# Kernel optimization log

Hardware: AMD Instinct MI355X
Metric: run time of the kernel (lower is better)

Reference implementation:

```python
import jax, jax.numpy as jnp
import numpy as np

TARGET_LEN = 288
HIDDEN = 128
INPUT_SIZE = 7
OUT_SIZE = 3  # len(quantiles)
BATCH = 1024
SEQ = 288


def _lstm_cell(x_t, h, c, Wih, Whh, b):
    # PyTorch LSTM gate order: i, f, g, o; z: (B, 4H)
    z = x_t @ Wih.T + h @ Whh.T + b
    i, f, g, o = jnp.split(z, 4, axis=-1)
    c_new = jax.nn.sigmoid(f) * c + jax.nn.sigmoid(i) * jnp.tanh(g)
    h_new = jax.nn.sigmoid(o) * jnp.tanh(c_new)
    return h_new, c_new


def setup_inputs() -> dict:
    key = jax.random.key(0)
    ks = jax.random.split(key, 11)
    s = 0.08  # ~ 1/sqrt(hidden), matches torch LSTM uniform init scale
    return {
        "x": jax.random.normal(ks[0], (BATCH, SEQ, INPUT_SIZE), jnp.float32),
        "enc_Wih": jax.random.normal(ks[1], (4 * HIDDEN, INPUT_SIZE), jnp.float32) * s,
        "enc_Whh": jax.random.normal(ks[2], (4 * HIDDEN, HIDDEN), jnp.float32) * s,
        "enc_bih": jax.random.normal(ks[3], (4 * HIDDEN,), jnp.float32) * s,
        "enc_bhh": jax.random.normal(ks[4], (4 * HIDDEN,), jnp.float32) * s,
        "dec_Wih": jax.random.normal(ks[5], (4 * HIDDEN, OUT_SIZE), jnp.float32) * s,
        "dec_Whh": jax.random.normal(ks[6], (4 * HIDDEN, HIDDEN), jnp.float32) * s,
        "dec_bih": jax.random.normal(ks[7], (4 * HIDDEN,), jnp.float32) * s,
        "dec_bhh": jax.random.normal(ks[8], (4 * HIDDEN,), jnp.float32) * s,
        "out_W": jax.random.normal(ks[9], (OUT_SIZE, HIDDEN), jnp.float32) * s,
        "out_b": jax.random.normal(ks[10], (OUT_SIZE,), jnp.float32) * s,
    }


def reference(x, enc_Wih, enc_Whh, enc_bih, enc_bhh,
              dec_Wih, dec_Whh, dec_bih, dec_bhh, out_W, out_b):
    B = x.shape[0]
    H = enc_Whh.shape[1]
    b_enc = enc_bih + enc_bhh
    b_dec = dec_bih + dec_bhh

    # ----- encoder LSTM over the input sequence -----
    def enc_step(carry, x_t):
        h, c = carry
        h, c = _lstm_cell(x_t, h, c, enc_Wih, enc_Whh, b_enc)
        return (h, c), None

    h0 = jnp.zeros((B, H), x.dtype)
    (h_enc, c_enc), _ = jax.lax.scan(enc_step, (h0, h0), jnp.swapaxes(x, 0, 1))

    # returned state, so every step restarts from (h_enc, c_enc); only the
    # previous output (quantiles) feeds back. Dropout is identity (eval). -----
    def dec_step(y_prev, _):
        h, _c = _lstm_cell(y_prev, h_enc, c_enc, dec_Wih, dec_Whh, b_dec)
        y = h @ out_W.T + out_b  # (B, OUT_SIZE)
        return y, y

    y0 = jnp.zeros((B, out_W.shape[0]), x.dtype)
    _, ys = jax.lax.scan(dec_step, y0, None, length=TARGET_LEN)  # (T, B, O)
    return jnp.swapaxes(ys, 0, 1)  # (B, TARGET_LEN, OUT_SIZE)
```

## Files before the change

### kernel.cpp

```cpp
#include <hip/hip_runtime.h>

#define SEQ 288
#define INP 7
#define HID 128
#define TLEN 288
#define OUTD 3
#define XW (SEQ * INP)

typedef _Float16 f16x8 __attribute__((ext_vector_type(8)));
typedef float f32x4 __attribute__((ext_vector_type(4)));

#define NLOG2E  (-1.4426950408889634f)
#define N2LOG2E (-2.8853900817779268f)

__device__ __forceinline__ float exp2_fast(float x) {
#if __has_builtin(__builtin_amdgcn_exp2f)
    return __builtin_amdgcn_exp2f(x);
#else
    return __expf(x * 0.69314718056f);
#endif
}
__device__ __forceinline__ float sig2(float zp) {
    return __builtin_amdgcn_rcpf(1.0f + exp2_fast(zp));
}
__device__ __forceinline__ float tanh2(float zp) {
    return 2.0f * __builtin_amdgcn_rcpf(1.0f + exp2_fast(zp)) - 1.0f;
}

template<int CTRL, int RM>
__device__ __forceinline__ float dpp_add(float v) {
    int t = __builtin_amdgcn_update_dpp(0, __float_as_int(v), CTRL, RM, 0xF, true);
    return v + __int_as_float(t);
}
__device__ __forceinline__ float wave_sum(float v) {
    v = dpp_add<0xB1, 0xF>(v);
    v = dpp_add<0x4E, 0xF>(v);
    v = dpp_add<0x124, 0xF>(v);
    v = dpp_add<0x128, 0xF>(v);
    v = dpp_add<0x142, 0xA>(v);
    v = dpp_add<0x143, 0xC>(v);
    return __int_as_float(__builtin_amdgcn_readlane(__float_as_int(v), 63));
}

__device__ __forceinline__ float sel4(f32x4 s, bool m1, bool m2) {
    float a = m1 ? s[1] : s[0];
    float b = m1 ? s[3] : s[2];
    return m2 ? b : a;
}

__global__ __launch_bounds__(512, 2)
void enc_dec_kernel(const float* __restrict__ x,
                    const float* __restrict__ eWih, const float* __restrict__ eWhh,
                    const float* __restrict__ ebih, const float* __restrict__ ebhh,
                    const float* __restrict__ dWih, const float* __restrict__ dWhh,
                    const float* __restrict__ dbih, const float* __restrict__ dbhh,
                    const float* __restrict__ oW,  const float* __restrict__ ob,
                    float* __restrict__ out)
{
    __shared__ __align__(16) _Float16 hbuf[2][4][4][40];
    __shared__ __align__(16) _Float16 xf16[SEQ + 1][4][8];
    __shared__ float zbl[4][4][HID];
    __shared__ float cl[4][HID];

    const int tid  = threadIdx.x;
    const int wave = tid >> 6;
    const int lane = tid & 63;
    const int col  = lane & 15;
    const int grp  = lane >> 4;
    const int u    = wave * 16 + col;
    const int bb   = grp;
    const int b0   = blockIdx.x * 4;
    const bool m1  = (grp & 1) != 0;
    const bool m2  = (grp & 2) != 0;

    const float GS[4] = {NLOG2E, NLOG2E, N2LOG2E, NLOG2E};

    {
        _Float16* hb = &hbuf[0][0][0][0];
        for (int i = tid; i < 2 * 4 * 4 * 40; i += 512) hb[i] = (_Float16)0.f;
        _Float16* xp = &xf16[SEQ][0][0];
        if (tid < 32) xp[tid] = (_Float16)0.f;
    }
    for (int i = tid; i < 4 * XW; i += 512) {
        int b = i / XW, r = i % XW;
        int t = r / INP, j = r % INP;
        xf16[t][b][j] = (_Float16)x[(size_t)(b0 + b) * XW + r];
    }
    for (int i = tid; i < SEQ * 4; i += 512)
        xf16[i >> 2][i & 3][7] = (_Float16)1.0f;

    f16x8 wfrag[4][5];
    #pragma unroll
    for (int gt = 0; gt < 4; ++gt) {
        const int row = gt * HID + u;
        const float gs = GS[gt];
        #pragma unroll
        for (int kc = 0; kc < 4; ++kc) {
            const float* wr = eWhh + (size_t)row * HID + kc * 32 + grp * 8;
            f16x8 wf;
            #pragma unroll
            for (int e = 0; e < 8; ++e) wf[e] = (_Float16)(gs * wr[e]);
            wfrag[gt][kc] = wf;
        }
        {
            f16x8 wf;
            #pragma unroll
            for (int e = 0; e < 8; ++e) {
                int j = grp * 8 + e;
                float v = 0.f;
                if (j < INP)       v = eWih[(size_t)row * INP + j];
                else if (j == 7)   v = ebih[row] + ebhh[row];
                wf[e] = (_Float16)(gs * v);
            }
            wfrag[gt][4] = wf;
        }
    }

    __syncthreads();

    float cc = 0.f;
    const f32x4 zero = (f32x4){0.f, 0.f, 0.f, 0.f};

    f32x4 accX[4];
    {
        f16x8 ax0 = *(const f16x8*)&xf16[0][col & 3][0];
        #pragma unroll
        for (int gt = 0; gt < 4; ++gt)
            accX[gt] = __builtin_amdgcn_mfma_f32_16x16x32_f16(ax0, wfrag[gt][4], zero, 0, 0, 0);
    }

    #define ENC_STEP(T, CUR, NXT)                                                     \
    {                                                                                 \
        f16x8 af0 = *(const f16x8*)&hbuf[CUR][0][col & 3][grp * 8];                   \
        f16x8 af1 = *(const f16x8*)&hbuf[CUR][1][col & 3][grp * 8];                   \
        f16x8 af2 = *(const f16x8*)&hbuf[CUR][2][col & 3][grp * 8];                   \
        f16x8 af3 = *(const f16x8*)&hbuf[CUR][3][col & 3][grp * 8];                   \
        f32x4 acc[4];                                                                 \
        _Pragma("unroll")                                                             \
        for (int gt = 0; gt < 4; ++gt) {                                              \
            acc[gt] = __builtin_amdgcn_mfma_f32_16x16x32_f16(af0, wfrag[gt][0], accX[gt], 0, 0, 0); \
            acc[gt] = __builtin_amdgcn_mfma_f32_16x16x32_f16(af1, wfrag[gt][1], acc[gt], 0, 0, 0);  \
            acc[gt] = __builtin_amdgcn_mfma_f32_16x16x32_f16(af2, wfrag[gt][2], acc[gt], 0, 0, 0);  \
            acc[gt] = __builtin_amdgcn_mfma_f32_16x16x32_f16(af3, wfrag[gt][3], acc[gt], 0, 0, 0);  \
        }                                                                             \
        f16x8 axn = *(const f16x8*)&xf16[(T) + 1][col & 3][0];                        \
        _Pragma("unroll")                                                             \
        for (int gt = 0; gt < 4; ++gt)                                                \
            accX[gt] = __builtin_amdgcn_mfma_f32_16x16x32_f16(axn, wfrag[gt][4], zero, 0, 0, 0);    \
        float zi = sel4(acc[0], m1, m2);                                              \
        float zf = sel4(acc[1], m1, m2);                                              \
        float zg = sel4(acc[2], m1, m2);                                              \
        float zo = sel4(acc[3], m1, m2);                                              \
        float si = sig2(zi);                                                          \
        float sf = sig2(zf);                                                          \
        float tg = tanh2(zg);                                                         \
        float so = sig2(zo);                                                          \
        cc = sf * cc + si * tg;                                                       \
        float h = so * tanh2(cc * N2LOG2E);                                           \
        hbuf[NXT][u >> 5][bb][u & 31] = (_Float16)h;                                  \
        __syncthreads();                                                              \
    }

    for (int t = 0; t < SEQ; t += 2) {
        ENC_STEP(t, 0, 1)
        ENC_STEP(t + 1, 1, 0)
    }
    #undef ENC_STEP

    #pragma unroll
    for (int gt = 0; gt < 4; ++gt) {
        const int row = gt * HID + u;
        const float gs = GS[gt];
        #pragma unroll
        for (int kc = 0; kc < 4; ++kc) {
            const float* wr = dWhh + (size_t)row * HID + kc * 32 + grp * 8;
            f16x8 wf;
            #pragma unroll
            for (int e = 0; e < 8; ++e) wf[e] = (_Float16)(gs * wr[e]);
            wfrag[gt][kc] = wf;
        }
    }
    {
        f16x8 af0 = *(const f16x8*)&hbuf[0][0][col & 3][grp * 8];
        f16x8 af1 = *(const f16x8*)&hbuf[0][1][col & 3][grp * 8];
        f16x8 af2 = *(const f16x8*)&hbuf[0][2][col & 3][grp * 8];
        f16x8 af3 = *(const f16x8*)&hbuf[0][3][col & 3][grp * 8];
        #pragma unroll
        for (int gt = 0; gt < 4; ++gt) {
            float bd = GS[gt] * (dbih[gt * HID + u] + dbhh[gt * HID + u]);
            f32x4 acc = (f32x4){bd, bd, bd, bd};
            acc = __builtin_amdgcn_mfma_f32_16x16x32_f16(af0, wfrag[gt][0], acc, 0, 0, 0);
            acc = __builtin_amdgcn_mfma_f32_16x16x32_f16(af1, wfrag[gt][1], acc, 0, 0, 0);
            acc = __builtin_amdgcn_mfma_f32_16x16x32_f16(af2, wfrag[gt][2], acc, 0, 0, 0);
            acc = __builtin_amdgcn_mfma_f32_16x16x32_f16(af3, wfrag[gt][3], acc, 0, 0, 0);
            zbl[gt][bb][u] = sel4(acc, m1, m2);
        }
        cl[bb][u] = cc;
    }
    __syncthreads();

    if (wave >= 4) return;
    {
        const int b = wave;
        const int u0 = lane, u1 = 64 + lane;
        float zb0[4], zb1[4], wd0[4][3], wd1[4][3];
        #pragma unroll
        for (int gt = 0; gt < 4; ++gt) {
            zb0[gt] = zbl[gt][b][u0];
            zb1[gt] = zbl[gt][b][u1];
            #pragma unroll
            for (int j = 0; j < 3; ++j) {
                wd0[gt][j] = GS[gt] * dWih[(size_t)(gt * HID + u0) * 3 + j];
                wd1[gt][j] = GS[gt] * dWih[(size_t)(gt * HID + u1) * 3 + j];
            }
        }
        const float c0 = cl[b][u0], c1 = cl[b][u1];
        float ow0[3], ow1[3];
        #pragma unroll
        for (int j = 0; j < 3; ++j) {
            ow0[j] = oW[j * HID + u0];
            ow1[j] = oW[j * HID + u1];
        }
        const float ob0 = ob[0], ob1 = ob[1], ob2 = ob[2];

        float y0 = 0.f, y1 = 0.f, y2 = 0.f;
        float* orow = out + (size_t)(b0 + b) * (TLEN * OUTD);

        for (int t = 0; t < TLEN; ++t) {
            float z0[4], z1[4];
            #pragma unroll
            for (int gt = 0; gt < 4; ++gt) {
                z0[gt] = zb0[gt] + wd0[gt][0] * y0 + wd0[gt][1] * y1 + wd0[gt][2] * y2;
                z1[gt] = zb1[gt] + wd1[gt][0] * y0 + wd1[gt][1] * y1 + wd1[gt][2] * y2;
            }
            float si0 = sig2(z0[0]), sf0 = sig2(z0[1]);
            float tg0 = tanh2(z0[2]), so0 = sig2(z0[3]);
            float si1 = sig2(z1[0]), sf1 = sig2(z1[1]);
            float tg1 = tanh2(z1[2]), so1 = sig2(z1[3]);
            float cd0 = sf0 * c0 + si0 * tg0;
            float cd1 = sf1 * c1 + si1 * tg1;
            float hd0 = so0 * tanh2(cd0 * N2LOG2E);
            float hd1 = so1 * tanh2(cd1 * N2LOG2E);
            float p0 = ow0[0] * hd0 + ow1[0] * hd1;
            float p1 = ow0[1] * hd0 + ow1[1] * hd1;
            float p2 = ow0[2] * hd0 + ow1[2] * hd1;
            y0 = wave_sum(p0) + ob0;
            y1 = wave_sum(p1) + ob1;
            y2 = wave_sum(p2) + ob2;
            if (lane < 3)
                orow[t * OUTD + lane] = (lane == 0) ? y0 : (lane == 1) ? y1 : y2;
        }
    }
}

extern "C" void kernel_launch(void* const* d_in, const int* in_sizes, int n_in,
                              void* d_out, int out_size, void* d_ws, size_t ws_size,
                              hipStream_t stream) {
    (void)in_sizes; (void)n_in; (void)d_ws; (void)ws_size; (void)out_size;
    enc_dec_kernel<<<256, 512, 0, stream>>>(
        (const float*)d_in[0],
        (const float*)d_in[1], (const float*)d_in[2],
        (const float*)d_in[3], (const float*)d_in[4],
        (const float*)d_in[5], (const float*)d_in[6],
        (const float*)d_in[7], (const float*)d_in[8],
        (const float*)d_in[9], (const float*)d_in[10],
        (float*)d_out);
}
```

Baseline: 258.7 us.

## Split encoder MFMA batch into two independent half-batch chains per wave

The encoder recurrence now runs two independent MFMA accumulation chains per gate, each covering two batch rows (split into separate LDS buffers A and B), and interleaves them instead of one serial 4-deep chain over four batch rows. The aim is to hide MFMA dependency latency on the serial critical path of each timestep. The cost is double the MFMA instruction count and more LDS reads and accumulator registers, which may pressure the launch bound of two blocks per CU.

After: 360.0 us. 39.2% more time.

```diff
diff --git a/kernel.cpp b/kernel.cpp
--- a/kernel.cpp
+++ b/kernel.cpp
@@ -40,12 +40,6 @@
     v = dpp_add<0x142, 0xA>(v);
     v = dpp_add<0x143, 0xC>(v);
     return __int_as_float(__builtin_amdgcn_readlane(__float_as_int(v), 63));
-}
-
-__device__ __forceinline__ float sel4(f32x4 s, bool m1, bool m2) {
-    float a = m1 ? s[1] : s[0];
-    float b = m1 ? s[3] : s[2];
-    return m2 ? b : a;
 }
 
 __global__ __launch_bounds__(512, 2)
@@ -57,7 +51,8 @@
                     const float* __restrict__ oW,  const float* __restrict__ ob,
                     float* __restrict__ out)
 {
-    __shared__ __align__(16) _Float16 hbuf[2][4][4][40];
+    __shared__ __align__(16) _Float16 hbA[2 * 4 * 2 * 40];
+    __shared__ __align__(16) _Float16 hbB[2 * 4 * 2 * 40];
     __shared__ __align__(16) _Float16 xf16[SEQ + 1][4][8];
     __shared__ float zbl[4][4][HID];
     __shared__ float cl[4][HID];
@@ -67,20 +62,22 @@
     const int lane = tid & 63;
     const int col  = lane & 15;
     const int grp  = lane >> 4;
+    const int G    = lane >> 5;
+    const int bl   = (lane >> 4) & 1;
+    const int gb   = G * 2 + bl;
     const int u    = wave * 16 + col;
-    const int bb   = grp;
     const int b0   = blockIdx.x * 4;
-    const bool m1  = (grp & 1) != 0;
-    const bool m2  = (grp & 2) != 0;
+    const bool m1  = bl != 0;
+    const bool mG  = G != 0;
+
+    const int rbase = (col & 1) * 40 + grp * 8;
+    const int woff  = (u >> 5) * 80 + bl * 40 + (u & 31);
+    _Float16* hbase = G ? hbB : hbA;
 
     const float GS[4] = {NLOG2E, NLOG2E, N2LOG2E, NLOG2E};
 
-    {
-        _Float16* hb = &hbuf[0][0][0][0];
-        for (int i = tid; i < 2 * 4 * 4 * 40; i += 512) hb[i] = (_Float16)0.f;
-        _Float16* xp = &xf16[SEQ][0][0];
-        if (tid < 32) xp[tid] = (_Float16)0.f;
-    }
+    for (int i = tid; i < 2 * 4 * 2 * 40; i += 512) { hbA[i] = (_Float16)0.f; hbB[i] = (_Float16)0.f; }
+    if (tid < 32) (&xf16[SEQ][0][0])[tid] = (_Float16)0.f;
     for (int i = tid; i < 4 * XW; i += 512) {
         int b = i / XW, r = i % XW;
         int t = r / INP, j = r % INP;
@@ -121,44 +118,70 @@
     float cc = 0.f;
     const f32x4 zero = (f32x4){0.f, 0.f, 0.f, 0.f};
 
-    f32x4 accX[4];
+    f32x4 accXA[4], accXB[4];
     {
-        f16x8 ax0 = *(const f16x8*)&xf16[0][col & 3][0];
-        #pragma unroll
-        for (int gt = 0; gt < 4; ++gt)
-            accX[gt] = __builtin_amdgcn_mfma_f32_16x16x32_f16(ax0, wfrag[gt][4], zero, 0, 0, 0);
-    }
-
-    #define ENC_STEP(T, CUR, NXT)                                                     \
-    {                                                                                 \
-        f16x8 af0 = *(const f16x8*)&hbuf[CUR][0][col & 3][grp * 8];                   \
-        f16x8 af1 = *(const f16x8*)&hbuf[CUR][1][col & 3][grp * 8];                   \
-        f16x8 af2 = *(const f16x8*)&hbuf[CUR][2][col & 3][grp * 8];                   \
-        f16x8 af3 = *(const f16x8*)&hbuf[CUR][3][col & 3][grp * 8];                   \
-        f32x4 acc[4];                                                                 \
-        _Pragma("unroll")                                                             \
-        for (int gt = 0; gt < 4; ++gt) {                                              \
-            acc[gt] = __builtin_amdgcn_mfma_f32_16x16x32_f16(af0, wfrag[gt][0], accX[gt], 0, 0, 0); \
-            acc[gt] = __builtin_amdgcn_mfma_f32_16x16x32_f16(af1, wfrag[gt][1], acc[gt], 0, 0, 0);  \
-            acc[gt] = __builtin_amdgcn_mfma_f32_16x16x32_f16(af2, wfrag[gt][2], acc[gt], 0, 0, 0);  \
-            acc[gt] = __builtin_amdgcn_mfma_f32_16x16x32_f16(af3, wfrag[gt][3], acc[gt], 0, 0, 0);  \
-        }                                                                             \
-        f16x8 axn = *(const f16x8*)&xf16[(T) + 1][col & 3][0];                        \
-        _Pragma("unroll")                                                             \
-        for (int gt = 0; gt < 4; ++gt)                                                \
-            accX[gt] = __builtin_amdgcn_mfma_f32_16x16x32_f16(axn, wfrag[gt][4], zero, 0, 0, 0);    \
-        float zi = sel4(acc[0], m1, m2);                                              \
-        float zf = sel4(acc[1], m1, m2);                                              \
-        float zg = sel4(acc[2], m1, m2);                                              \
-        float zo = sel4(acc[3], m1, m2);                                              \
-        float si = sig2(zi);                                                          \
-        float sf = sig2(zf);                                                          \
-        float tg = tanh2(zg);                                                         \
-        float so = sig2(zo);                                                          \
-        cc = sf * cc + si * tg;                                                       \
-        float h = so * tanh2(cc * N2LOG2E);                                           \
-        hbuf[NXT][u >> 5][bb][u & 31] = (_Float16)h;                                  \
-        __syncthreads();                                                              \
+        f16x8 axA = *(const f16x8*)&xf16[0][col & 1][0];
+        f16x8 axB = *(const f16x8*)&xf16[0][2 + (col & 1)][0];
+        #pragma unroll
+        for (int gt = 0; gt < 4; ++gt) {
+            accXA[gt] = __builtin_amdgcn_mfma_f32_16x16x32_f16(axA, wfrag[gt][4], zero, 0, 0, 0);
+            accXB[gt] = __builtin_amdgcn_mfma_f32_16x16x32_f16(axB, wfrag[gt][4], zero, 0, 0, 0);
+        }
+    }
+
+    #define ENC_STEP(T, CUR, NXT)                                                      \
+    {                                                                                  \
+        f16x8 aA0 = *(const f16x8*)&hbA[(CUR)*320 + 0*80 + rbase];                     \
+        f16x8 aB0 = *(const f16x8*)&hbB[(CUR)*320 + 0*80 + rbase];                     \
+        f16x8 aA1 = *(const f16x8*)&hbA[(CUR)*320 + 1*80 + rbase];                     \
+        f16x8 aB1 = *(const f16x8*)&hbB[(CUR)*320 + 1*80 + rbase];                     \
+        f16x8 aA2 = *(const f16x8*)&hbA[(CUR)*320 + 2*80 + rbase];                     \
+        f16x8 aB2 = *(const f16x8*)&hbB[(CUR)*320 + 2*80 + rbase];                     \
+        f16x8 aA3 = *(const f16x8*)&hbA[(CUR)*320 + 3*80 + rbase];                     \
+        f16x8 aB3 = *(const f16x8*)&hbB[(CUR)*320 + 3*80 + rbase];                     \
+        f32x4 accA[4], accB[4];                                                        \
+        _Pragma("unroll")                                                              \
+        for (int gt = 0; gt < 4; ++gt) {                                               \
+            accA[gt] = __builtin_amdgcn_mfma_f32_16x16x32_f16(aA0, wfrag[gt][0], accXA[gt], 0, 0, 0); \
+            accB[gt] = __builtin_amdgcn_mfma_f32_16x16x32_f16(aB0, wfrag[gt][0], accXB[gt], 0, 0, 0); \
+        }                                                                              \
+        _Pragma("unroll")                                                              \
+        for (int gt = 0; gt < 4; ++gt) {                                               \
+            accA[gt] = __builtin_amdgcn_mfma_f32_16x16x32_f16(aA1, wfrag[gt][1], accA[gt], 0, 0, 0);  \
+            accB[gt] = __builtin_amdgcn_mfma_f32_16x16x32_f16(aB1, wfrag[gt][1], accB[gt], 0, 0, 0);  \
+        }                                                                              \
+        _Pragma("unroll")                                                              \
+        for (int gt = 0; gt < 4; ++gt) {                                               \
+            accA[gt] = __builtin_amdgcn_mfma_f32_16x16x32_f16(aA2, wfrag[gt][2], accA[gt], 0, 0, 0);  \
+            accB[gt] = __builtin_amdgcn_mfma_f32_16x16x32_f16(aB2, wfrag[gt][2], accB[gt], 0, 0, 0);  \
+        }                                                                              \
+        _Pragma("unroll")                                                              \
+        for (int gt = 0; gt < 4; ++gt) {                                               \
+            accA[gt] = __builtin_amdgcn_mfma_f32_16x16x32_f16(aA3, wfrag[gt][3], accA[gt], 0, 0, 0);  \
+            accB[gt] = __builtin_amdgcn_mfma_f32_16x16x32_f16(aB3, wfrag[gt][3], accB[gt], 0, 0, 0);  \
+        }                                                                              \
+        f16x8 axA = *(const f16x8*)&xf16[(T) + 1][col & 1][0];                         \
+        f16x8 axB = *(const f16x8*)&xf16[(T) + 1][2 + (col & 1)][0];                   \
+        _Pragma("unroll")                                                              \
+        for (int gt = 0; gt < 4; ++gt) {                                               \
+            accXA[gt] = __builtin_amdgcn_mfma_f32_16x16x32_f16(axA, wfrag[gt][4], zero, 0, 0, 0);     \
+            accXB[gt] = __builtin_amdgcn_mfma_f32_16x16x32_f16(axB, wfrag[gt][4], zero, 0, 0, 0);     \
+        }                                                                              \
+        float z[4];                                                                    \
+        _Pragma("unroll")                                                              \
+        for (int gt = 0; gt < 4; ++gt) {                                               \
+            float za = m1 ? accA[gt][1] : accA[gt][0];                                 \
+            float zv = m1 ? accB[gt][1] : accB[gt][0];                                 \
+            z[gt] = mG ? zv : za;                                                      \
+        }                                                                              \
+        float si = sig2(z[0]);                                                         \
+        float sf = sig2(z[1]);                                                         \
+        float tg = tanh2(z[2]);                                                        \
+        float so = sig2(z[3]);                                                         \
+        cc = sf * cc + si * tg;                                                        \
+        float h = so * tanh2(cc * N2LOG2E);                                            \
+        hbase[(NXT)*320 + woff] = (_Float16)h;                                         \
+        __syncthreads();                                                               \
     }
 
     for (int t = 0; t < SEQ; t += 2) {
@@ -181,21 +204,32 @@
         }
     }
     {
-        f16x8 af0 = *(const f16x8*)&hbuf[0][0][col & 3][grp * 8];
-        f16x8 af1 = *(const f16x8*)&hbuf[0][1][col & 3][grp * 8];
-        f16x8 af2 = *(const f16x8*)&hbuf[0][2][col & 3][grp * 8];
-        f16x8 af3 = *(const f16x8*)&hbuf[0][3][col & 3][grp * 8];
+        f16x8 aA0 = *(const f16x8*)&hbA[0*80 + rbase];
+        f16x8 aB0 = *(const f16x8*)&hbB[0*80 + rbase];
+        f16x8 aA1 = *(const f16x8*)&hbA[1*80 + rbase];
+        f16x8 aB1 = *(const f16x8*)&hbB[1*80 + rbase];
+        f16x8 aA2 = *(const f16x8*)&hbA[2*80 + rbase];
+        f16x8 aB2 = *(const f16x8*)&hbB[2*80 + rbase];
+        f16x8 aA3 = *(const f16x8*)&hbA[3*80 + rbase];
+        f16x8 aB3 = *(const f16x8*)&hbB[3*80 + rbase];
         #pragma unroll
         for (int gt = 0; gt < 4; ++gt) {
             float bd = GS[gt] * (dbih[gt * HID + u] + dbhh[gt * HID + u]);
-            f32x4 acc = (f32x4){bd, bd, bd, bd};
-            acc = __builtin_amdgcn_mfma_f32_16x16x32_f16(af0, wfrag[gt][0], acc, 0, 0, 0);
-            acc = __builtin_amdgcn_mfma_f32_16x16x32_f16(af1, wfrag[gt][1], acc, 0, 0, 0);
-            acc = __builtin_amdgcn_mfma_f32_16x16x32_f16(af2, wfrag[gt][2], acc, 0, 0, 0);
-            acc = __builtin_amdgcn_mfma_f32_16x16x32_f16(af3, wfrag[gt][3], acc, 0, 0, 0);
-            zbl[gt][bb][u] = sel4(acc, m1, m2);
-        }
-        cl[bb][u] = cc;
+            f32x4 aA = (f32x4){bd, bd, bd, bd};
+            f32x4 aB = aA;
+            aA = __builtin_amdgcn_mfma_f32_16x16x32_f16(aA0, wfrag[gt][0], aA, 0, 0, 0);
+            aB = __builtin_amdgcn_mfma_f32_16x16x32_f16(aB0, wfrag[gt][0], aB, 0, 0, 0);
+            aA = __builtin_amdgcn_mfma_f32_16x16x32_f16(aA1, wfrag[gt][1], aA, 0, 0, 0);
+            aB = __builtin_amdgcn_mfma_f32_16x16x32_f16(aB1, wfrag[gt][1], aB, 0, 0, 0);
+            aA = __builtin_amdgcn_mfma_f32_16x16x32_f16(aA2, wfrag[gt][2], aA, 0, 0, 0);
+            aB = __builtin_amdgcn_mfma_f32_16x16x32_f16(aB2, wfrag[gt][2], aB, 0, 0, 0);
+            aA = __builtin_amdgcn_mfma_f32_16x16x32_f16(aA3, wfrag[gt][3], aA, 0, 0, 0);
+            aB = __builtin_amdgcn_mfma_f32_16x16x32_f16(aB3, wfrag[gt][3], aB, 0, 0, 0);
+            float za = m1 ? aA[1] : aA[0];
+            float zv = m1 ? aB[1] : aB[0];
+            zbl[gt][gb][u] = mG ? zv : za;
+        }
+        cl[gb][u] = cc;
     }
     __syncthreads();
 
```

## Batch input projection over four timesteps and remap MFMA rows to drop selects

Applied to the files above, without the earlier changes.

The input-projection MFMA now runs once per four encoder steps, packing four timesteps into the A-operand rows so each MFMA yields x-contributions for all four steps. The hidden-state A rows are remapped (col>>2 instead of col&3), so each lane's batch result lands in acc[0] and the per-gate 4-way select is removed. This cuts the input MFMAs per step from four to one amortized and removes select instructions on the serial critical path. The price is that the four matrix MFMAs per gate now start from zero rather than from a precomputed accumulator, which adds a VALU add per gate, and the accumulator-to-lane mapping has to be correct for the transposed layout.

Measured after the change: 247.1 us (median of 2 runs). 4.5% less time.

```diff
diff --git a/kernel.cpp b/kernel.cpp
--- a/kernel.cpp
+++ b/kernel.cpp
@@ -40,12 +40,6 @@
     v = dpp_add<0x142, 0xA>(v);
     v = dpp_add<0x143, 0xC>(v);
     return __int_as_float(__builtin_amdgcn_readlane(__float_as_int(v), 63));
-}
-
-__device__ __forceinline__ float sel4(f32x4 s, bool m1, bool m2) {
-    float a = m1 ? s[1] : s[0];
-    float b = m1 ? s[3] : s[2];
-    return m2 ? b : a;
 }
 
 __global__ __launch_bounds__(512, 2)
@@ -58,7 +52,7 @@
                     float* __restrict__ out)
 {
     __shared__ __align__(16) _Float16 hbuf[2][4][4][40];
-    __shared__ __align__(16) _Float16 xf16[SEQ + 1][4][8];
+    __shared__ __align__(16) _Float16 xf16[SEQ][4][8];
     __shared__ float zbl[4][4][HID];
     __shared__ float cl[4][HID];
 
@@ -70,16 +64,12 @@
     const int u    = wave * 16 + col;
     const int bb   = grp;
     const int b0   = blockIdx.x * 4;
-    const bool m1  = (grp & 1) != 0;
-    const bool m2  = (grp & 2) != 0;
 
     const float GS[4] = {NLOG2E, NLOG2E, N2LOG2E, NLOG2E};
 
     {
         _Float16* hb = &hbuf[0][0][0][0];
         for (int i = tid; i < 2 * 4 * 4 * 40; i += 512) hb[i] = (_Float16)0.f;
-        _Float16* xp = &xf16[SEQ][0][0];
-        if (tid < 32) xp[tid] = (_Float16)0.f;
     }
     for (int i = tid; i < 4 * XW; i += 512) {
         int b = i / XW, r = i % XW;
@@ -121,49 +111,42 @@
     float cc = 0.f;
     const f32x4 zero = (f32x4){0.f, 0.f, 0.f, 0.f};
 
-    f32x4 accX[4];
-    {
-        f16x8 ax0 = *(const f16x8*)&xf16[0][col & 3][0];
-        #pragma unroll
-        for (int gt = 0; gt < 4; ++gt)
-            accX[gt] = __builtin_amdgcn_mfma_f32_16x16x32_f16(ax0, wfrag[gt][4], zero, 0, 0, 0);
-    }
-
-    #define ENC_STEP(T, CUR, NXT)                                                     \
+    #define ENC_STEP(DT, CUR, NXT)                                                    \
     {                                                                                 \
-        f16x8 af0 = *(const f16x8*)&hbuf[CUR][0][col & 3][grp * 8];                   \
-        f16x8 af1 = *(const f16x8*)&hbuf[CUR][1][col & 3][grp * 8];                   \
-        f16x8 af2 = *(const f16x8*)&hbuf[CUR][2][col & 3][grp * 8];                   \
-        f16x8 af3 = *(const f16x8*)&hbuf[CUR][3][col & 3][grp * 8];                   \
+        f16x8 af0 = *(const f16x8*)&hbuf[CUR][0][col >> 2][grp * 8];                  \
+        f16x8 af1 = *(const f16x8*)&hbuf[CUR][1][col >> 2][grp * 8];                  \
+        f16x8 af2 = *(const f16x8*)&hbuf[CUR][2][col >> 2][grp * 8];                  \
+        f16x8 af3 = *(const f16x8*)&hbuf[CUR][3][col >> 2][grp * 8];                  \
         f32x4 acc[4];                                                                 \
         _Pragma("unroll")                                                             \
         for (int gt = 0; gt < 4; ++gt) {                                              \
-            acc[gt] = __builtin_amdgcn_mfma_f32_16x16x32_f16(af0, wfrag[gt][0], accX[gt], 0, 0, 0); \
-            acc[gt] = __builtin_amdgcn_mfma_f32_16x16x32_f16(af1, wfrag[gt][1], acc[gt], 0, 0, 0);  \
-            acc[gt] = __builtin_amdgcn_mfma_f32_16x16x32_f16(af2, wfrag[gt][2], acc[gt], 0, 0, 0);  \
-            acc[gt] = __builtin_amdgcn_mfma_f32_16x16x32_f16(af3, wfrag[gt][3], acc[gt], 0, 0, 0);  \
+            acc[gt] = __builtin_amdgcn_mfma_f32_16x16x32_f16(af0, wfrag[gt][0], zero,    0, 0, 0); \
+            acc[gt] = __builtin_amdgcn_mfma_f32_16x16x32_f16(af1, wfrag[gt][1], acc[gt], 0, 0, 0); \
+            acc[gt] = __builtin_amdgcn_mfma_f32_16x16x32_f16(af2, wfrag[gt][2], acc[gt], 0, 0, 0); \
+            acc[gt] = __builtin_amdgcn_mfma_f32_16x16x32_f16(af3, wfrag[gt][3], acc[gt], 0, 0, 0); \
         }                                                                             \
-        f16x8 axn = *(const f16x8*)&xf16[(T) + 1][col & 3][0];                        \
-        _Pragma("unroll")                                                             \
-        for (int gt = 0; gt < 4; ++gt)                                                \
-            accX[gt] = __builtin_amdgcn_mfma_f32_16x16x32_f16(axn, wfrag[gt][4], zero, 0, 0, 0);    \
-        float zi = sel4(acc[0], m1, m2);                                              \
-        float zf = sel4(acc[1], m1, m2);                                              \
-        float zg = sel4(acc[2], m1, m2);                                              \
-        float zo = sel4(acc[3], m1, m2);                                              \
-        float si = sig2(zi);                                                          \
-        float sf = sig2(zf);                                                          \
-        float tg = tanh2(zg);                                                         \
-        float so = sig2(zo);                                                          \
+        float si = sig2(acc[0][0] + zxp[0][DT]);                                      \
+        float sf = sig2(acc[1][0] + zxp[1][DT]);                                      \
+        float tg = tanh2(acc[2][0] + zxp[2][DT]);                                     \
+        float so = sig2(acc[3][0] + zxp[3][DT]);                                      \
         cc = sf * cc + si * tg;                                                       \
         float h = so * tanh2(cc * N2LOG2E);                                           \
         hbuf[NXT][u >> 5][bb][u & 31] = (_Float16)h;                                  \
         __syncthreads();                                                              \
     }
 
-    for (int t = 0; t < SEQ; t += 2) {
-        ENC_STEP(t, 0, 1)
-        ENC_STEP(t + 1, 1, 0)
+    for (int t4 = 0; t4 < SEQ; t4 += 4) {
+        f32x4 zxp[4];
+        {
+            f16x8 axp = *(const f16x8*)&xf16[t4 + (col & 3)][col >> 2][0];
+            #pragma unroll
+            for (int gt = 0; gt < 4; ++gt)
+                zxp[gt] = __builtin_amdgcn_mfma_f32_16x16x32_f16(axp, wfrag[gt][4], zero, 0, 0, 0);
+        }
+        ENC_STEP(0, 0, 1)
+        ENC_STEP(1, 1, 0)
+        ENC_STEP(2, 0, 1)
+        ENC_STEP(3, 1, 0)
     }
     #undef ENC_STEP
 
@@ -181,10 +164,10 @@
         }
     }
     {
-        f16x8 af0 = *(const f16x8*)&hbuf[0][0][col & 3][grp * 8];
-        f16x8 af1 = *(const f16x8*)&hbuf[0][1][col & 3][grp * 8];
-        f16x8 af2 = *(const f16x8*)&hbuf[0][2][col & 3][grp * 8];
-        f16x8 af3 = *(const f16x8*)&hbuf[0][3][col & 3][grp * 8];
+        f16x8 af0 = *(const f16x8*)&hbuf[0][0][col >> 2][grp * 8];
+        f16x8 af1 = *(const f16x8*)&hbuf[0][1][col >> 2][grp * 8];
+        f16x8 af2 = *(const f16x8*)&hbuf[0][2][col >> 2][grp * 8];
+        f16x8 af3 = *(const f16x8*)&hbuf[0][3][col >> 2][grp * 8];
         #pragma unroll
         for (int gt = 0; gt < 4; ++gt) {
             float bd = GS[gt] * (dbih[gt * HID + u] + dbhh[gt * HID + u]);
@@ -193,7 +176,7 @@
             acc = __builtin_amdgcn_mfma_f32_16x16x32_f16(af1, wfrag[gt][1], acc, 0, 0, 0);
             acc = __builtin_amdgcn_mfma_f32_16x16x32_f16(af2, wfrag[gt][2], acc, 0, 0, 0);
             acc = __builtin_amdgcn_mfma_f32_16x16x32_f16(af3, wfrag[gt][3], acc, 0, 0, 0);
-            zbl[gt][bb][u] = sel4(acc, m1, m2);
+            zbl[gt][bb][u] = acc[0];
         }
         cl[bb][u] = cc;
     }
```
